# Kernel optimization log

Hardware: AMD Instinct MI355X
Metric: run time of the kernel (lower is better)

The kernel has to match this reference:

```python
import jax, jax.numpy as jnp
import numpy as np

VX, VY, VZ = 0.2, 0.2, 4.0
PCR = (0.0, -40.0, -3.0, 70.4, 40.0, 1.0)
X_OFF = VX / 2 + PCR[0]
Y_OFF = VY / 2 + PCR[1]
Z_OFF = VZ / 2 + PCR[2]
BN_EPS = 1e-3
N_POINTS = 600000
N_VOXELS = 60000
CANVAS_X, CANVAS_Y = 352, 400  # (70.4-0)/0.2, (40-(-40))/0.2


def setup_inputs() -> dict:
    key = jax.random.key(0)
    ks = jax.random.split(key, 8)
    rng = np.random.default_rng(0)
    # pick N_VOXELS distinct occupied voxels on the BEV canvas
    lin = rng.permutation(CANVAS_X * CANVAS_Y)[:N_VOXELS]
    inv = rng.integers(0, N_VOXELS, size=N_POINTS)
    inv[:N_VOXELS] = np.arange(N_VOXELS)  # guarantee every voxel occupied
    pv = lin[inv]
    coors = np.zeros((N_POINTS, 4), np.int32)  # (batch, z, y, x)
    coors[:, 3] = pv % CANVAS_X
    coors[:, 2] = pv // CANVAS_X
    # point features: xyz inside point cloud range + intensity
    px = jax.random.uniform(ks[0], (N_POINTS,), minval=PCR[0], maxval=PCR[3])
    py = jax.random.uniform(ks[1], (N_POINTS,), minval=PCR[1], maxval=PCR[4])
    pz = jax.random.uniform(ks[2], (N_POINTS,), minval=PCR[2], maxval=PCR[5])
    pi = jax.random.uniform(ks[3], (N_POINTS,))
    features = jnp.stack([px, py, pz, pi], axis=1)
    return {
        'features': features,
        'w0': jax.random.normal(ks[4], (10, 64)) * 0.3,
        'g0': jnp.ones((64,)),
        'b0': jnp.zeros((64,)),
        'w1': jax.random.normal(ks[5], (128, 128)) * 0.08,
        'g1': jnp.ones((128,)),
        'b1': jnp.zeros((128,)),
        'coors': jnp.asarray(coors),
        'unq_inv': jnp.asarray(inv.astype(np.int32)),
        'num_voxels': N_VOXELS,
    }


def _bn_relu(x, g, b):
    # BN1d training-mode forward: biased batch stats, eps=1e-3
    mu = jnp.mean(x, axis=0)
    var = jnp.mean(jnp.square(x - mu), axis=0)
    return jax.nn.relu((x - mu) * jax.lax.rsqrt(var + BN_EPS) * g + b)


def reference(features, w0, g0, b0, w1, g1, b1, coors, unq_inv, num_voxels):
    n = features.shape[0]
    cf = coors.astype(features.dtype)
    # cluster center: scatter-mean of point features per voxel, gathered back
    vsum = jax.ops.segment_sum(features, unq_inv, num_segments=num_voxels)
    cnt = jax.ops.segment_sum(jnp.ones((n, 1), features.dtype), unq_inv,
                              num_segments=num_voxels)
    voxel_mean = vsum / jnp.maximum(cnt, 1.0)
    f_cluster = features[:, :3] - voxel_mean[unq_inv][:, :3]
    # offset to voxel center (coors layout: batch, z, y, x)
    f_center = jnp.stack([
        features[:, 0] - (cf[:, 3] * VX + X_OFF),
        features[:, 1] - (cf[:, 2] * VY + Y_OFF),
        features[:, 2] - (cf[:, 1] * VZ + Z_OFF),
    ], axis=1)
    x = jnp.concatenate([features, f_cluster, f_center], axis=1)  # [N,10]
    # VFE layer 0 + scatter-max pool + gather-concat
    p0 = _bn_relu(x @ w0, g0, b0)                                  # [N,64]
    v0 = jax.ops.segment_max(p0, unq_inv, num_segments=num_voxels)
    x1 = jnp.concatenate([p0, v0[unq_inv]], axis=1)                # [N,128]
    # VFE layer 1 + final scatter-max pool
    p1 = _bn_relu(x1 @ w1, g1, b1)                                 # [N,128]
    voxel_feats = jax.ops.segment_max(p1, unq_inv, num_segments=num_voxels)
    return voxel_feats  # [M,128]
```

## Files before the change

kernel.cpp:

```cpp
#include <hip/hip_runtime.h>
#include <hip/hip_bf16.h>


typedef __attribute__((ext_vector_type(8))) short bf16x8;
typedef __attribute__((ext_vector_type(4))) float f32x4;
typedef __attribute__((ext_vector_type(4))) int i32x4;
typedef unsigned short u16;
typedef unsigned int u32;

#define GRIDV 1172
#define RSP 72
#define SCB 2048

__device__ __forceinline__ float bf2f(u16 u) { return __uint_as_float(((u32)u) << 16); }
__device__ __forceinline__ u16 f2bfbits(float f) {
  __hip_bfloat16 h = __float2bfloat16(f);
  return __builtin_bit_cast(u16, h);
}
__device__ __forceinline__ float ldf(const void* p, int i, int flag) {
  return flag ? bf2f(((const u16*)p)[i]) : ((const float*)p)[i];
}
__device__ __forceinline__ u32 encf(float f) {
  u32 b = __float_as_uint(f);
  return b ^ ((u32)(((int)b) >> 31) | 0x80000000u);
}
__device__ __forceinline__ float decf(u32 k) {
  u32 b = (k & 0x80000000u) ? (k ^ 0x80000000u) : ~k;
  return __uint_as_float(b);
}

__device__ __forceinline__ void compute_x(
    int p, const void* __restrict__ feat, const int4* __restrict__ coors4,
    const int* __restrict__ inv, const float* __restrict__ vsum,
    const unsigned* __restrict__ vcnt, int flag, float x[10]) {
  float px, py, pz, pi;
  if (flag) {
    ushort4 f = ((const ushort4*)feat)[p];
    px = bf2f(f.x); py = bf2f(f.y); pz = bf2f(f.z); pi = bf2f(f.w);
  } else {
    float4 f = ((const float4*)feat)[p];
    px = f.x; py = f.y; pz = f.z; pi = f.w;
  }
  int4 c = coors4[p];
  int v = inv[p];
  unsigned cn = vcnt[v];
  float cnt = (float)(cn ? cn : 1u);
  float mx = vsum[3 * v + 0] / cnt;
  float my = vsum[3 * v + 1] / cnt;
  float mz = vsum[3 * v + 2] / cnt;
  x[0] = px; x[1] = py; x[2] = pz; x[3] = pi;
  x[4] = px - mx; x[5] = py - my; x[6] = pz - mz;
  x[7] = px - ((float)c.w * 0.2f + 0.1f);
  x[8] = py - ((float)c.z * 0.2f - 39.9f);
  x[9] = pz - ((float)c.y * 4.0f - 1.0f);
}

__global__ void k_probe(const u32* __restrict__ g0bits, int* __restrict__ flag) {
  if (threadIdx.x == 0 && blockIdx.x == 0)
    flag[0] = (g0bits[0] == 0x3F800000u) ? 0 : 1;
}

__global__ __launch_bounds__(256) void k_pre(
    const void* __restrict__ w0p, const void* __restrict__ w1p,
    const void* __restrict__ g1p,
    u16* __restrict__ w0t, u16* __restrict__ w1t, u32* __restrict__ gsign,
    float4* __restrict__ z4a, long nza4,
    float4* __restrict__ keysws, float4* __restrict__ doutp, long nzk4,
    const int* __restrict__ flagp) {
  const int t = threadIdx.x;
  const int flag = flagp[0];
  if (blockIdx.x == 0) {
    for (int i = t; i < 2048; i += 256) {
      int c = i >> 5, k = i & 31;
      w0t[i] = (k < 10) ? f2bfbits(ldf(w0p, k * 64 + c, flag)) : (u16)0;
    }
    for (int i = t; i < 16384; i += 256) {
      int c = i >> 7, k = i & 127;
      w1t[i] = f2bfbits(ldf(w1p, k * 128 + c, flag));
    }
    if (t < 128) gsign[t] = (ldf(g1p, t, flag) < 0.f) ? 0xFFFFFFFFu : 0u;
  } else {
    float4* keys4 = flag ? keysws : doutp;
    const long total = nza4 + nzk4;
    const long nth = (long)(gridDim.x - 1) * 256;
    const float4 z = {0.f, 0.f, 0.f, 0.f};
    for (long i = (long)(blockIdx.x - 1) * 256 + t; i < total; i += nth) {
      if (i < nza4) z4a[i] = z; else keys4[i - nza4] = z;
    }
  }
}

__global__ __launch_bounds__(256) void k_scatter(
    const void* __restrict__ feat, const int* __restrict__ inv,
    float* __restrict__ vsum, unsigned* __restrict__ vcnt,
    const int* __restrict__ flagp, int n) {
  const int flag = flagp[0];
  const int stride = gridDim.x * blockDim.x;
  for (int p = blockIdx.x * blockDim.x + threadIdx.x; p < n; p += stride) {
    float px, py, pz;
    if (flag) {
      ushort4 f = ((const ushort4*)feat)[p];
      px = bf2f(f.x); py = bf2f(f.y); pz = bf2f(f.z);
    } else {
      float4 f = ((const float4*)feat)[p];
      px = f.x; py = f.y; pz = f.z;
    }
    int v = inv[p];
    atomicAdd(&vsum[3 * v + 0], px);
    atomicAdd(&vsum[3 * v + 1], py);
    atomicAdd(&vsum[3 * v + 2], pz);
    atomicAdd(&vcnt[v], 1u);
  }
}

__global__ __launch_bounds__(256) void k_scanA(const unsigned* __restrict__ vcnt,
                                               unsigned* __restrict__ bsum, int M) {
  __shared__ unsigned sh[4];
  const int t = threadIdx.x;
  long base = (long)blockIdx.x * SCB;
  unsigned s = 0;
  for (int i = t; i < SCB; i += 256) {
    long idx = base + i;
    s += (idx < M) ? vcnt[idx] : 0u;
  }
  #pragma unroll
  for (int off = 1; off < 64; off <<= 1) s += __shfl_xor(s, off);
  if ((t & 63) == 0) sh[t >> 6] = s;
  __syncthreads();
  if (t == 0) bsum[blockIdx.x] = sh[0] + sh[1] + sh[2] + sh[3];
}

__global__ __launch_bounds__(256) void k_scanB(const unsigned* __restrict__ bsum,
                                               unsigned* __restrict__ boff, int nb) {
  __shared__ unsigned sh[256];
  const int t = threadIdx.x;
  unsigned loc[8];
  unsigned s = 0;
  #pragma unroll
  for (int j = 0; j < 8; ++j) {
    int i = t * 8 + j;
    loc[j] = (i < nb) ? bsum[i] : 0u;
    s += loc[j];
  }
  sh[t] = s; __syncthreads();
  for (int off = 1; off < 256; off <<= 1) {
    unsigned add = (t >= off) ? sh[t - off] : 0u;
    __syncthreads();
    sh[t] += add;
    __syncthreads();
  }
  unsigned excl = sh[t] - s;
  #pragma unroll
  for (int j = 0; j < 8; ++j) {
    int i = t * 8 + j;
    if (i < nb) { boff[i] = excl; excl += loc[j]; }
  }
}

__global__ __launch_bounds__(256) void k_scanC(const unsigned* __restrict__ vcnt,
                                               const unsigned* __restrict__ boff,
                                               unsigned* __restrict__ voff, int M) {
  __shared__ unsigned sh[256];
  const int t = threadIdx.x;
  long base = (long)blockIdx.x * SCB;
  unsigned loc[8];
  unsigned s = 0;
  #pragma unroll
  for (int j = 0; j < 8; ++j) {
    long i = base + t * 8 + j;
    loc[j] = (i < M) ? vcnt[i] : 0u;
    s += loc[j];
  }
  sh[t] = s; __syncthreads();
  for (int off = 1; off < 256; off <<= 1) {
    unsigned add = (t >= off) ? sh[t - off] : 0u;
    __syncthreads();
    sh[t] += add;
    __syncthreads();
  }
  unsigned excl = sh[t] - s + boff[blockIdx.x];
  #pragma unroll
  for (int j = 0; j < 8; ++j) {
    long i = base + t * 8 + j;
    if (i < M) { voff[i] = excl; excl += loc[j]; }
  }
}

__global__ __launch_bounds__(256) void k_fillx(
    const void* __restrict__ feat, const int4* __restrict__ coors4,
    const int* __restrict__ inv, const float* __restrict__ vsum,
    const unsigned* __restrict__ vcnt, const unsigned* __restrict__ voff,
    unsigned* __restrict__ wcur, u32* __restrict__ xpk,
    float* __restrict__ stat0acc, const int* __restrict__ flagp, int n) {
  const int flag = flagp[0];
  float acc[65];
  #pragma unroll
  for (int j = 0; j < 65; ++j) acc[j] = 0.f;
  const int t = threadIdx.x;
  const int stride = gridDim.x * blockDim.x;
  for (int p = blockIdx.x * blockDim.x + t; p < n; p += stride) {
    float x[10];
    compute_x(p, feat, coors4, inv, vsum, vcnt, flag, x);
    const int v = inv[p];
    int k = 0;
    #pragma unroll
    for (int a = 0; a < 10; ++a) acc[k++] += x[a];
    #pragma unroll
    for (int a = 0; a < 10; ++a) {
      #pragma unroll
      for (int b = a; b < 10; ++b) acc[k++] += x[a] * x[b];
    }
    u32 u[5];
    #pragma unroll
    for (int j = 0; j < 5; ++j)
      u[j] = (u32)f2bfbits(x[2 * j]) | ((u32)f2bfbits(x[2 * j + 1]) << 16);
    const unsigned pos = voff[v] + atomicAdd(&wcur[v], 1u);
    uint4* dst = (uint4*)(xpk + (long)pos * 8);
    uint4 q0 = {u[0], u[1], u[2], u[3]};
    uint4 q1 = {u[4], (u32)v, 0u, 0u};
    dst[0] = q0;
    dst[1] = q1;
  }
  __shared__ float red[65];
  if (t < 65) red[t] = 0.f;
  __syncthreads();
  const int lane = t & 63;
  #pragma unroll
  for (int j = 0; j < 65; ++j) {
    float s = acc[j];
    #pragma unroll
    for (int off = 1; off < 64; off <<= 1) s += __shfl_xor(s, off);
    if (lane == 0) atomicAdd(&red[j], s);
  }
  __syncthreads();
  if (t < 65) atomicAdd(&stat0acc[t], red[t]);
}

__global__ void k_bn0fin(const float* __restrict__ stat0acc,
                         const void* __restrict__ w0p,
                         const void* __restrict__ g0p,
                         const void* __restrict__ b0p,
                         float* __restrict__ a0, float* __restrict__ c0,
                         const int* __restrict__ flagp, int n) {
  const int flag = flagp[0];
  __shared__ float tot[65];
  const int t = threadIdx.x;
  if (t < 65) tot[t] = stat0acc[t];
  __syncthreads();
  if (t < 64) {
    const float invN = 1.0f / (float)n;
    float w[10];
    #pragma unroll
    for (int i = 0; i < 10; ++i) w[i] = ldf(w0p, i * 64 + t, flag);
    float mu = 0.f;
    #pragma unroll
    for (int i = 0; i < 10; ++i) mu += tot[i] * w[i];
    mu *= invN;
    float e2 = 0.f;
    int k = 10;
    #pragma unroll
    for (int a = 0; a < 10; ++a) {
      #pragma unroll
      for (int b = a; b < 10; ++b) {
        float term = tot[k++] * invN * w[a] * w[b];
        e2 += (a == b) ? term : 2.0f * term;
      }
    }
    float var = fmaxf(e2 - mu * mu, 0.f);
    float rs = 1.0f / sqrtf(var + 1e-3f);
    float aa = ldf(g0p, t, flag) * rs;
    a0[t] = aa;
    c0[t] = ldf(b0p, t, flag) - mu * aa;
  }
}

__device__ __forceinline__ bf16x8 l0frag(const u32* __restrict__ xpk,
                                         long grow, long n, int kg) {
  i32x4 ai = {0, 0, 0, 0};
  if (grow < n) {
    const u32* rp = xpk + grow * 8;
    if (kg == 0) {
      uint4 q = *(const uint4*)rp;
      ai[0] = (int)q.x; ai[1] = (int)q.y; ai[2] = (int)q.z; ai[3] = (int)q.w;
    } else if (kg == 1) {
      ai[0] = (int)rp[4];
    }
  }
  return __builtin_bit_cast(bf16x8, ai);
}

__global__ __launch_bounds__(256) void k_l0vox(
    const u32* __restrict__ xpk, const u16* __restrict__ w0t,
    const float* __restrict__ a0, const float* __restrict__ c0,
    float* __restrict__ v0, int n, int nst, int M) {
  __shared__ float l0stg[4 * 1056];
  __shared__ int vxs[256];
  const int t = threadIdx.x, lane = t & 63, w = t >> 6;
  const int cl = lane & 15, kg = lane >> 4;
  float* fst = l0stg + w * 1056;
  bf16x8 bw[4];
  float al[4], be[4];
  #pragma unroll
  for (int ct = 0; ct < 4; ++ct) {
    bw[ct] = *(const bf16x8*)(w0t + (16 * ct + cl) * 32 + 8 * kg);
    al[ct] = a0[16 * ct + cl];
    be[ct] = c0[16 * ct + cl];
  }
  for (int st = blockIdx.x; st < nst; st += gridDim.x) {
    const long jb = (long)st * 256;
    vxs[t] = (jb + t < n) ? (int)xpk[(jb + t) * 8 + 5] : M;
    int curv = -2;
    float m = 0.f;
    bool edge = true;
    #pragma unroll
    for (int mt = 0; mt < 4; ++mt) {
      const long grow = jb + 64 * w + 16 * mt + cl;
      bf16x8 av = l0frag(xpk, grow, n, kg);
      f32x4 acc[4];
      #pragma unroll
      for (int ct = 0; ct < 4; ++ct) {
        f32x4 z = {0.f, 0.f, 0.f, 0.f};
        acc[ct] = __builtin_amdgcn_mfma_f32_16x16x32_bf16(av, bw[ct], z, 0, 0, 0);
      }
      #pragma unroll
      for (int ct = 0; ct < 4; ++ct)
        #pragma unroll
        for (int i2 = 0; i2 < 4; ++i2)
          fst[(4 * kg + i2) * 66 + 16 * ct + cl] =
              fmaxf(fmaf(acc[ct][i2], al[ct], be[ct]), 0.f);
      const int rbase = 64 * w + 16 * mt;
      for (int r = 0; r < 16; ++r) {
        int v = vxs[rbase + r];
        float a = fst[r * 66 + lane];
        if (v != curv) {
          if (curv >= 0 && curv < M) {
            if (edge) atomicMax((int*)&v0[(long)curv * 64 + lane], __float_as_int(m));
            else      v0[(long)curv * 64 + lane] = m;
          }
          if (curv != -2) edge = false;
          curv = v; m = a;
        } else m = fmaxf(m, a);
      }
    }
    if (curv >= 0 && curv < M)
      atomicMax((int*)&v0[(long)curv * 64 + lane], __float_as_int(m));
  }
}

__device__ __forceinline__ bf16x8 pack8(float4 a, float4 b) {
  bf16x8 r;
  r[0] = (short)f2bfbits(a.x); r[1] = (short)f2bfbits(a.y);
  r[2] = (short)f2bfbits(a.z); r[3] = (short)f2bfbits(a.w);
  r[4] = (short)f2bfbits(b.x); r[5] = (short)f2bfbits(b.y);
  r[6] = (short)f2bfbits(b.z); r[7] = (short)f2bfbits(b.w);
  return r;
}

__global__ __launch_bounds__(256, 2) void k_vfe1vox(
    const u32* __restrict__ xpk, const u16* __restrict__ w0t,
    const float* __restrict__ a0, const float* __restrict__ c0,
    const u16* __restrict__ w1t, const u32* __restrict__ gsign,
    const float* __restrict__ v0,
    u32* __restrict__ keysws, u32* __restrict__ doutk,
    float* __restrict__ stat1acc,
    const int* __restrict__ flagp, int n, int nst, int M) {
  const int flag = flagp[0];
  u32* keys = flag ? keysws : doutk;
  __shared__ u16 stg[256 * RSP];
  __shared__ int vxs[256];
  __shared__ float sred[128], qred[128];
  const int t = threadIdx.x, lane = t & 63, w = t >> 6;
  const int cl = lane & 15, kg = lane >> 4;
  u32* yst = (u32*)(stg + 4608 * w);
  bf16x8 bw[4];
  float al[4], be[4];
  u32 gs[8];
  #pragma unroll
  for (int ct = 0; ct < 4; ++ct) {
    bw[ct] = *(const bf16x8*)(w0t + (16 * ct + cl) * 32 + 8 * kg);
    al[ct] = a0[16 * ct + cl];
    be[ct] = c0[16 * ct + cl];
  }
  #pragma unroll
  for (int ct = 0; ct < 8; ++ct) gs[ct] = gsign[16 * ct + cl];
  float ssum[8], ssq[8];
  #pragma unroll
  for (int jj = 0; jj < 8; ++jj) { ssum[jj] = 0.f; ssq[jj] = 0.f; }
  const f32x4 fz = {0.f, 0.f, 0.f, 0.f};

  for (int st = blockIdx.x; st < nst; st += gridDim.x) {
    const long jb = (long)st * 256;
    vxs[t] = (jb + t < n) ? (int)xpk[(jb + t) * 8 + 5] : M;
    #pragma unroll
    for (int mt = 0; mt < 4; ++mt) {
      const long grow = jb + 64 * w + 16 * mt + cl;
      bf16x8 av = l0frag(xpk, grow, n, kg);
      f32x4 acc0[4];
      #pragma unroll
      for (int ct = 0; ct < 4; ++ct)
        acc0[ct] = __builtin_amdgcn_mfma_f32_16x16x32_bf16(av, bw[ct], fz, 0, 0, 0);
      #pragma unroll
      for (int ct = 0; ct < 4; ++ct) {
        const int c = 16 * ct + cl;
        #pragma unroll
        for (int i2 = 0; i2 < 4; ++i2) {
          const int rloc = 64 * w + 16 * mt + 4 * kg + i2;
          float y = fmaxf(fmaf(acc0[ct][i2], al[ct], be[ct]), 0.f);
          if (jb + rloc >= n) y = 0.f;
          stg[rloc * RSP + c] = f2bfbits(y);
        }
      }
    }
    bf16x8 afr[2][2][4];
    #pragma unroll
    for (int mth = 0; mth < 2; ++mth)
      #pragma unroll
      for (int mtl = 0; mtl < 2; ++mtl) {
        const int rloc = 64 * w + 32 * mth + 16 * mtl + cl;
        afr[mth][mtl][0] = *(const bf16x8*)&stg[rloc * RSP + 8 * kg];
        afr[mth][mtl][1] = *(const bf16x8*)&stg[rloc * RSP + 32 + 8 * kg];
        const int vv = vxs[rloc];
        const float* vr = v0 + (long)vv * 64;
        float4 f0 = *(const float4*)(vr + 8 * kg);
        float4 f1 = *(const float4*)(vr + 8 * kg + 4);
        float4 f2 = *(const float4*)(vr + 32 + 8 * kg);
        float4 f3 = *(const float4*)(vr + 32 + 8 * kg + 4);
        afr[mth][mtl][2] = pack8(f0, f1);
        afr[mth][mtl][3] = pack8(f2, f3);
      }
    int curv = -2;
    u32 m0 = 0, m1 = 0;
    bool edge = true;
    #pragma unroll
    for (int mth = 0; mth < 2; ++mth) {
      f32x4 acc[2][8];
      #pragma unroll
      for (int ct = 0; ct < 8; ++ct) {
        const u16* wr = w1t + (16 * ct + cl) * 128 + 8 * kg;
        bf16x8 b0 = *(const bf16x8*)(wr);
        bf16x8 b1 = *(const bf16x8*)(wr + 32);
        bf16x8 b2 = *(const bf16x8*)(wr + 64);
        bf16x8 b3 = *(const bf16x8*)(wr + 96);
        #pragma unroll
        for (int mtl = 0; mtl < 2; ++mtl) {
          f32x4 a = fz;
          a = __builtin_amdgcn_mfma_f32_16x16x32_bf16(afr[mth][mtl][0], b0, a, 0, 0, 0);
          a = __builtin_amdgcn_mfma_f32_16x16x32_bf16(afr[mth][mtl][1], b1, a, 0, 0, 0);
          a = __builtin_amdgcn_mfma_f32_16x16x32_bf16(afr[mth][mtl][2], b2, a, 0, 0, 0);
          a = __builtin_amdgcn_mfma_f32_16x16x32_bf16(afr[mth][mtl][3], b3, a, 0, 0, 0);
          acc[mtl][ct] = a;
        }
      }
      #pragma unroll
      for (int mtl = 0; mtl < 2; ++mtl) {
        #pragma unroll
        for (int ct = 0; ct < 8; ++ct) {
          #pragma unroll
          for (int i2 = 0; i2 < 4; ++i2) {
            float y = acc[mtl][ct][i2];
            ssum[ct] += y; ssq[ct] += y * y;
            yst[(4 * kg + i2) * 130 + 16 * ct + cl] = encf(y) ^ gs[ct];
          }
        }
        const int rbase = 64 * w + 32 * mth + 16 * mtl;
        for (int r = 0; r < 16; ++r) {
          int v = vxs[rbase + r];
          u32 a0r = yst[r * 130 + lane], a1r = yst[r * 130 + 64 + lane];
          if (v != curv) {
            if (curv >= 0 && curv < M) {
              u32* row = keys + (long)curv * 128;
              if (edge) { atomicMax(&row[lane], m0); atomicMax(&row[64 + lane], m1); }
              else      { row[lane] = m0; row[64 + lane] = m1; }
            }
            if (curv != -2) edge = false;
            curv = v; m0 = a0r; m1 = a1r;
          } else { m0 = max(m0, a0r); m1 = max(m1, a1r); }
        }
      }
    }
    if (curv >= 0 && curv < M) {
      u32* row = keys + (long)curv * 128;
      atomicMax(&row[lane], m0); atomicMax(&row[64 + lane], m1);
    }
  }
  if (t < 128) { sred[t] = 0.f; qred[t] = 0.f; }
  __syncthreads();
  #pragma unroll
  for (int ct = 0; ct < 8; ++ct) {
    float s = ssum[ct], q = ssq[ct];
    s += __shfl_xor(s, 16); s += __shfl_xor(s, 32);
    q += __shfl_xor(q, 16); q += __shfl_xor(q, 32);
    if (lane < 16) {
      atomicAdd(&sred[ct * 16 + cl], s);
      atomicAdd(&qred[ct * 16 + cl], q);
    }
  }
  __syncthreads();
  if (t < 128) {
    atomicAdd(&stat1acc[t], sred[t]);
    atomicAdd(&stat1acc[128 + t], qred[t]);
  }
}

__global__ void k_bn1fin(const float* __restrict__ stat1acc,
                         const void* __restrict__ g1p,
                         const void* __restrict__ b1p,
                         float* __restrict__ a1, float* __restrict__ c1,
                         const int* __restrict__ flagp, int n) {
  const int flag = flagp[0];
  const int c = threadIdx.x;
  float s = stat1acc[c];
  float q = stat1acc[128 + c];
  const float invN = 1.0f / (float)n;
  float mu = s * invN;
  float var = fmaxf(q * invN - mu * mu, 0.f);
  float rs = 1.0f / sqrtf(var + 1e-3f);
  float aa = ldf(g1p, c, flag) * rs;
  a1[c] = aa;
  c1[c] = ldf(b1p, c, flag) - mu * aa;
}

__global__ __launch_bounds__(256) void k_fin(
    const u32* __restrict__ keysws, u32* __restrict__ doutk,
    const float* __restrict__ a1, const float* __restrict__ c1,
    const u32* __restrict__ gsign, void* __restrict__ dout,
    const int* __restrict__ flagp, int m32) {
  const int flag = flagp[0];
  const uint4* src = (const uint4*)(flag ? keysws : doutk);
  const int stride = gridDim.x * blockDim.x;
  for (int i = blockIdx.x * blockDim.x + threadIdx.x; i < m32; i += stride) {
    uint4 k = src[i];
    const int cb = (i * 4) & 127;
    float z0 = fmaxf(fmaf(decf(k.x ^ gsign[cb + 0]), a1[cb + 0], c1[cb + 0]), 0.f);
    float z1 = fmaxf(fmaf(decf(k.y ^ gsign[cb + 1]), a1[cb + 1], c1[cb + 1]), 0.f);
    float z2 = fmaxf(fmaf(decf(k.z ^ gsign[cb + 2]), a1[cb + 2], c1[cb + 2]), 0.f);
    float z3 = fmaxf(fmaf(decf(k.w ^ gsign[cb + 3]), a1[cb + 3], c1[cb + 3]), 0.f);
    if (flag) {
      ushort4 o;
      o.x = f2bfbits(z0); o.y = f2bfbits(z1); o.z = f2bfbits(z2); o.w = f2bfbits(z3);
      ((ushort4*)dout)[i] = o;
    } else {
      float4 o = {z0, z1, z2, z3};
      ((float4*)dout)[i] = o;
    }
  }
}

extern "C" void kernel_launch(void* const* d_in, const int* in_sizes, int n_in,
                              void* d_out, int out_size, void* d_ws, size_t ws_size,
                              hipStream_t stream) {
  (void)n_in; (void)ws_size;
  const int n = in_sizes[0] / 4;
  const int M = out_size / 128;
  const int nst = (n + 255) >> 8;
  const int nb = (M + SCB - 1) / SCB;
  if (n <= 0 || M <= 0) return;

  const void* feat = d_in[0];
  const void* w0p = d_in[1];
  const void* g0p = d_in[2];
  const void* b0p = d_in[3];
  const void* w1p = d_in[4];
  const void* g1p = d_in[5];
  const void* b1p = d_in[6];
  const int4* coors4 = (const int4*)d_in[7];
  const int* inv = (const int*)d_in[8];

  char* wsb = (char*)d_ws;
  long off = 0;
  auto alloc = [&](long bytes) -> void* {
    void* p = wsb + off;
    off = (off + bytes + 255) & ~255L;
    return p;
  };
  int* flagp = (int*)alloc(256);
  float* a0 = (float*)alloc(256);
  float* c0 = (float*)alloc(256);
  float* a1 = (float*)alloc(512);
  float* c1 = (float*)alloc(512);
  u32* gsign = (u32*)alloc(512);
  u16* w0t = (u16*)alloc(2048 * 2);
  u16* w1t = (u16*)alloc(16384 * 2);
  unsigned* bsum = (unsigned*)alloc(2048 * 4);
  unsigned* boff = (unsigned*)alloc(2048 * 4);
  unsigned* voff = (unsigned*)alloc((long)M * 4);
  u32* xpk = (u32*)alloc((long)nst * 256 * 32);
  const long nza = 384L + 3L * M + M + (long)(M + 1) * 64 + M;
  float* zbase = (float*)alloc(((nza + 3) / 4) * 16);
  float* stat0acc = zbase;
  float* stat1acc = zbase + 80;
  float* vsum = zbase + 384;
  unsigned* vcnt = (unsigned*)(vsum + 3L * M);
  float* v0 = (float*)(vcnt + M);
  unsigned* wcur = (unsigned*)(v0 + (long)(M + 1) * 64);
  u32* keysws = (u32*)alloc((long)M * 128 * 4);

  hipLaunchKernelGGL(k_probe, dim3(1), dim3(64), 0, stream, (const u32*)g0p, flagp);
  hipLaunchKernelGGL(k_pre, dim3(2048), dim3(256), 0, stream,
                     w0p, w1p, g1p, w0t, w1t, gsign,
                     (float4*)zbase, (nza + 3) / 4,
                     (float4*)keysws, (float4*)d_out, (long)M * 32, flagp);
  hipLaunchKernelGGL(k_scatter, dim3(1024), dim3(256), 0, stream, feat, inv, vsum, vcnt, flagp, n);
  hipLaunchKernelGGL(k_scanA, dim3(nb), dim3(256), 0, stream, vcnt, bsum, M);
  hipLaunchKernelGGL(k_scanB, dim3(1), dim3(256), 0, stream, bsum, boff, nb);
  hipLaunchKernelGGL(k_scanC, dim3(nb), dim3(256), 0, stream, vcnt, boff, voff, M);
  hipLaunchKernelGGL(k_fillx, dim3(1024), dim3(256), 0, stream,
                     feat, coors4, inv, vsum, vcnt, voff, wcur, xpk, stat0acc, flagp, n);
  hipLaunchKernelGGL(k_bn0fin, dim3(1), dim3(128), 0, stream,
                     stat0acc, w0p, g0p, b0p, a0, c0, flagp, n);
  hipLaunchKernelGGL(k_l0vox, dim3(GRIDV), dim3(256), 0, stream,
                     xpk, w0t, a0, c0, v0, n, nst, M);
  hipLaunchKernelGGL(k_vfe1vox, dim3(GRIDV), dim3(256), 0, stream,
                     xpk, w0t, a0, c0, w1t, gsign, v0,
                     keysws, (u32*)d_out, stat1acc, flagp, n, nst, M);
  hipLaunchKernelGGL(k_bn1fin, dim3(1), dim3(128), 0, stream,
                     stat1acc, g1p, b1p, a1, c1, flagp, n);
  hipLaunchKernelGGL(k_fin, dim3(1024), dim3(256), 0, stream,
                     keysws, (u32*)d_out, a1, c1, gsign, d_out, flagp, M * 32);
}
```

Measured before the change: 435.6 us.

## Replace float atomic voxel sums with sorted gather and merge block-edge maxima in shared memory

The per-point float atomicAdd scatter for voxel sums is replaced by a count histogram, a fill pass that builds a sorted point list plus a point-to-position map, and a per-voxel gather that sums features without atomics. fillx reuses the precomputed positions instead of doing a second atomic slot claim. The two VFE kernels now give each wave a fixed run of contiguous 64-row segments instead of grid-striding over 256-row tiles. Each wave's boundary voxels are merged across the block in shared memory, so fewer global atomicMax calls are needed, and vfe1vox occupancy is raised to 3 blocks. The cost is two extra launches and extra workspace traffic, and the per-voxel serial gather loop is unbalanced because voxel point counts vary.

```diff
diff --git a/kernel.cpp b/kernel.cpp
--- a/kernel.cpp
+++ b/kernel.cpp
@@ -8,9 +8,11 @@
 typedef unsigned short u16;
 typedef unsigned int u32;
 
-#define GRIDV 1172
 #define RSP 72
 #define SCB 2048
+#define WPB 4
+#define SPW0 2
+#define SPW1 3
 
 __device__ __forceinline__ float bf2f(u16 u) { return __uint_as_float(((u32)u) << 16); }
 __device__ __forceinline__ u16 f2bfbits(float f) {
@@ -90,27 +92,11 @@
   }
 }
 
-__global__ __launch_bounds__(256) void k_scatter(
-    const void* __restrict__ feat, const int* __restrict__ inv,
-    float* __restrict__ vsum, unsigned* __restrict__ vcnt,
-    const int* __restrict__ flagp, int n) {
-  const int flag = flagp[0];
+__global__ __launch_bounds__(256) void k_hist(const int* __restrict__ inv,
+                                              unsigned* __restrict__ vcnt, int n) {
   const int stride = gridDim.x * blockDim.x;
-  for (int p = blockIdx.x * blockDim.x + threadIdx.x; p < n; p += stride) {
-    float px, py, pz;
-    if (flag) {
-      ushort4 f = ((const ushort4*)feat)[p];
-      px = bf2f(f.x); py = bf2f(f.y); pz = bf2f(f.z);
-    } else {
-      float4 f = ((const float4*)feat)[p];
-      px = f.x; py = f.y; pz = f.z;
-    }
-    int v = inv[p];
-    atomicAdd(&vsum[3 * v + 0], px);
-    atomicAdd(&vsum[3 * v + 1], py);
-    atomicAdd(&vsum[3 * v + 2], pz);
-    atomicAdd(&vcnt[v], 1u);
-  }
+  for (int p = blockIdx.x * blockDim.x + threadIdx.x; p < n; p += stride)
+    atomicAdd(&vcnt[inv[p]], 1u);
 }
 
 __global__ __launch_bounds__(256) void k_scanA(const unsigned* __restrict__ vcnt,
@@ -186,12 +172,49 @@
   }
 }
 
+__global__ __launch_bounds__(256) void k_fill(
+    const int* __restrict__ inv, const unsigned* __restrict__ voff,
+    unsigned* __restrict__ wcur, int* __restrict__ plist,
+    unsigned* __restrict__ pt2pos, int n) {
+  const int stride = gridDim.x * blockDim.x;
+  for (int p = blockIdx.x * blockDim.x + threadIdx.x; p < n; p += stride) {
+    int v = inv[p];
+    unsigned pos = voff[v] + atomicAdd(&wcur[v], 1u);
+    plist[pos] = p;
+    pt2pos[p] = pos;
+  }
+}
+
+__global__ __launch_bounds__(256) void k_vsum(
+    const void* __restrict__ feat, const int* __restrict__ plist,
+    const unsigned* __restrict__ voff, const unsigned* __restrict__ vcnt,
+    float* __restrict__ vsum, const int* __restrict__ flagp, int M) {
+  const int flag = flagp[0];
+  const int v = blockIdx.x * 256 + threadIdx.x;
+  if (v >= M) return;
+  const unsigned o = voff[v], c = vcnt[v];
+  float sx = 0.f, sy = 0.f, sz = 0.f;
+  for (unsigned j = 0; j < c; ++j) {
+    int pid = plist[o + j];
+    if (flag) {
+      ushort4 f = ((const ushort4*)feat)[pid];
+      sx += bf2f(f.x); sy += bf2f(f.y); sz += bf2f(f.z);
+    } else {
+      float4 f = ((const float4*)feat)[pid];
+      sx += f.x; sy += f.y; sz += f.z;
+    }
+  }
+  vsum[3 * v + 0] = sx;
+  vsum[3 * v + 1] = sy;
+  vsum[3 * v + 2] = sz;
+}
+
 __global__ __launch_bounds__(256) void k_fillx(
     const void* __restrict__ feat, const int4* __restrict__ coors4,
     const int* __restrict__ inv, const float* __restrict__ vsum,
-    const unsigned* __restrict__ vcnt, const unsigned* __restrict__ voff,
-    unsigned* __restrict__ wcur, u32* __restrict__ xpk,
-    float* __restrict__ stat0acc, const int* __restrict__ flagp, int n) {
+    const unsigned* __restrict__ vcnt, const unsigned* __restrict__ pt2pos,
+    u32* __restrict__ xpk, float* __restrict__ stat0acc,
+    const int* __restrict__ flagp, int n) {
   const int flag = flagp[0];
   float acc[65];
   #pragma unroll
@@ -214,7 +237,7 @@
     #pragma unroll
     for (int j = 0; j < 5; ++j)
       u[j] = (u32)f2bfbits(x[2 * j]) | ((u32)f2bfbits(x[2 * j + 1]) << 16);
-    const unsigned pos = voff[v] + atomicAdd(&wcur[v], 1u);
+    const unsigned pos = pt2pos[p];
     uint4* dst = (uint4*)(xpk + (long)pos * 8);
     uint4 q0 = {u[0], u[1], u[2], u[3]};
     uint4 q1 = {u[4], (u32)v, 0u, 0u};
@@ -292,9 +315,11 @@
 __global__ __launch_bounds__(256) void k_l0vox(
     const u32* __restrict__ xpk, const u16* __restrict__ w0t,
     const float* __restrict__ a0, const float* __restrict__ c0,
-    float* __restrict__ v0, int n, int nst, int M) {
+    float* __restrict__ v0, long n, long nseg, int M) {
   __shared__ float l0stg[4 * 1056];
-  __shared__ int vxs[256];
+  __shared__ int vxsw[4][64];
+  __shared__ float pval[8][64];
+  __shared__ int pvox[8];
   const int t = threadIdx.x, lane = t & 63, w = t >> 6;
   const int cl = lane & 15, kg = lane >> 4;
   float* fst = l0stg + w * 1056;
@@ -306,15 +331,17 @@
     al[ct] = a0[16 * ct + cl];
     be[ct] = c0[16 * ct + cl];
   }
-  for (int st = blockIdx.x; st < nst; st += gridDim.x) {
-    const long jb = (long)st * 256;
-    vxs[t] = (jb + t < n) ? (int)xpk[(jb + t) * 8 + 5] : M;
-    int curv = -2;
-    float m = 0.f;
-    bool edge = true;
+  int curv = -2; float m = 0.f;
+  bool first = true; int fvox = -2; float fm = 0.f;
+  const long seg0 = ((long)blockIdx.x * WPB + w) * SPW0;
+  for (int s = 0; s < SPW0; ++s) {
+    const long seg = seg0 + s;
+    if (seg >= nseg) break;
+    const long jb = seg * 64;
+    vxsw[w][lane] = (jb + lane < n) ? (int)xpk[(jb + lane) * 8 + 5] : M;
     #pragma unroll
     for (int mt = 0; mt < 4; ++mt) {
-      const long grow = jb + 64 * w + 16 * mt + cl;
+      const long grow = jb + 16 * mt + cl;
       bf16x8 av = l0frag(xpk, grow, n, kg);
       f32x4 acc[4];
       #pragma unroll
@@ -328,22 +355,40 @@
         for (int i2 = 0; i2 < 4; ++i2)
           fst[(4 * kg + i2) * 66 + 16 * ct + cl] =
               fmaxf(fmaf(acc[ct][i2], al[ct], be[ct]), 0.f);
-      const int rbase = 64 * w + 16 * mt;
+      const int rb = 16 * mt;
       for (int r = 0; r < 16; ++r) {
-        int v = vxs[rbase + r];
+        int v = vxsw[w][rb + r];
         float a = fst[r * 66 + lane];
         if (v != curv) {
           if (curv >= 0 && curv < M) {
-            if (edge) atomicMax((int*)&v0[(long)curv * 64 + lane], __float_as_int(m));
-            else      v0[(long)curv * 64 + lane] = m;
+            if (first) { fvox = curv; fm = m; first = false; }
+            else v0[(long)curv * 64 + lane] = m;
           }
-          if (curv != -2) edge = false;
           curv = v; m = a;
         } else m = fmaxf(m, a);
       }
     }
-    if (curv >= 0 && curv < M)
-      atomicMax((int*)&v0[(long)curv * 64 + lane], __float_as_int(m));
+  }
+  if (lane == 0) { pvox[2 * w] = fvox; pvox[2 * w + 1] = curv; }
+  pval[2 * w][lane] = fm;
+  pval[2 * w + 1][lane] = m;
+  __syncthreads();
+  if (t < 64) {
+    int vox = -2; float val = 0.f; bool afirst = true;
+    for (int e = 0; e < 8; ++e) {
+      int ev = pvox[e];
+      if (ev < 0 || ev >= M) continue;
+      float evv = pval[e][t];
+      if (ev == vox) val = fmaxf(val, evv);
+      else {
+        if (vox >= 0) {
+          if (afirst) { atomicMax((int*)&v0[(long)vox * 64 + t], __float_as_int(val)); afirst = false; }
+          else v0[(long)vox * 64 + t] = val;
+        }
+        vox = ev; val = evv;
+      }
+    }
+    if (vox >= 0) atomicMax((int*)&v0[(long)vox * 64 + t], __float_as_int(val));
   }
 }
 
@@ -356,19 +401,21 @@
   return r;
 }
 
-__global__ __launch_bounds__(256, 2) void k_vfe1vox(
+__global__ __launch_bounds__(256, 3) void k_vfe1vox(
     const u32* __restrict__ xpk, const u16* __restrict__ w0t,
     const float* __restrict__ a0, const float* __restrict__ c0,
     const u16* __restrict__ w1t, const u32* __restrict__ gsign,
     const float* __restrict__ v0,
     u32* __restrict__ keysws, u32* __restrict__ doutk,
     float* __restrict__ stat1acc,
-    const int* __restrict__ flagp, int n, int nst, int M) {
+    const int* __restrict__ flagp, long n, long nseg, int M) {
   const int flag = flagp[0];
   u32* keys = flag ? keysws : doutk;
   __shared__ u16 stg[256 * RSP];
-  __shared__ int vxs[256];
+  __shared__ int vxsw[4][64];
   __shared__ float sred[128], qred[128];
+  __shared__ u32 pval[8][128];
+  __shared__ int pvox[8];
   const int t = threadIdx.x, lane = t & 63, w = t >> 6;
   const int cl = lane & 15, kg = lane >> 4;
   u32* yst = (u32*)(stg + 4608 * w);
@@ -388,12 +435,18 @@
   for (int jj = 0; jj < 8; ++jj) { ssum[jj] = 0.f; ssq[jj] = 0.f; }
   const f32x4 fz = {0.f, 0.f, 0.f, 0.f};
 
-  for (int st = blockIdx.x; st < nst; st += gridDim.x) {
-    const long jb = (long)st * 256;
-    vxs[t] = (jb + t < n) ? (int)xpk[(jb + t) * 8 + 5] : M;
+  int curv = -2; u32 m0 = 0, m1 = 0;
+  bool first = true; int fvox = -2; u32 fm0 = 0, fm1 = 0;
+  const long seg0 = ((long)blockIdx.x * WPB + w) * SPW1;
+
+  for (int s = 0; s < SPW1; ++s) {
+    const long seg = seg0 + s;
+    if (seg >= nseg) break;
+    const long jb = seg * 64;
+    vxsw[w][lane] = (jb + lane < n) ? (int)xpk[(jb + lane) * 8 + 5] : M;
     #pragma unroll
     for (int mt = 0; mt < 4; ++mt) {
-      const long grow = jb + 64 * w + 16 * mt + cl;
+      const long grow = jb + 16 * mt + cl;
       bf16x8 av = l0frag(xpk, grow, n, kg);
       f32x4 acc0[4];
       #pragma unroll
@@ -404,10 +457,10 @@
         const int c = 16 * ct + cl;
         #pragma unroll
         for (int i2 = 0; i2 < 4; ++i2) {
-          const int rloc = 64 * w + 16 * mt + 4 * kg + i2;
+          const int lr = 16 * mt + 4 * kg + i2;
           float y = fmaxf(fmaf(acc0[ct][i2], al[ct], be[ct]), 0.f);
-          if (jb + rloc >= n) y = 0.f;
-          stg[rloc * RSP + c] = f2bfbits(y);
+          if (jb + lr >= n) y = 0.f;
+          stg[(64 * w + lr) * RSP + c] = f2bfbits(y);
         }
       }
     }
@@ -416,10 +469,10 @@
     for (int mth = 0; mth < 2; ++mth)
       #pragma unroll
       for (int mtl = 0; mtl < 2; ++mtl) {
-        const int rloc = 64 * w + 32 * mth + 16 * mtl + cl;
-        afr[mth][mtl][0] = *(const bf16x8*)&stg[rloc * RSP + 8 * kg];
-        afr[mth][mtl][1] = *(const bf16x8*)&stg[rloc * RSP + 32 + 8 * kg];
-        const int vv = vxs[rloc];
+        const int lr = 32 * mth + 16 * mtl + cl;
+        afr[mth][mtl][0] = *(const bf16x8*)&stg[(64 * w + lr) * RSP + 8 * kg];
+        afr[mth][mtl][1] = *(const bf16x8*)&stg[(64 * w + lr) * RSP + 32 + 8 * kg];
+        const int vv = vxsw[w][lr];
         const float* vr = v0 + (long)vv * 64;
         float4 f0 = *(const float4*)(vr + 8 * kg);
         float4 f1 = *(const float4*)(vr + 8 * kg + 4);
@@ -428,9 +481,6 @@
         afr[mth][mtl][2] = pack8(f0, f1);
         afr[mth][mtl][3] = pack8(f2, f3);
       }
-    int curv = -2;
-    u32 m0 = 0, m1 = 0;
-    bool edge = true;
     #pragma unroll
     for (int mth = 0; mth < 2; ++mth) {
       f32x4 acc[2][8];
@@ -462,29 +512,46 @@
             yst[(4 * kg + i2) * 130 + 16 * ct + cl] = encf(y) ^ gs[ct];
           }
         }
-        const int rbase = 64 * w + 32 * mth + 16 * mtl;
+        const int rb = 32 * mth + 16 * mtl;
         for (int r = 0; r < 16; ++r) {
-          int v = vxs[rbase + r];
+          int v = vxsw[w][rb + r];
           u32 a0r = yst[r * 130 + lane], a1r = yst[r * 130 + 64 + lane];
           if (v != curv) {
             if (curv >= 0 && curv < M) {
-              u32* row = keys + (long)curv * 128;
-              if (edge) { atomicMax(&row[lane], m0); atomicMax(&row[64 + lane], m1); }
-              else      { row[lane] = m0; row[64 + lane] = m1; }
+              if (first) { fvox = curv; fm0 = m0; fm1 = m1; first = false; }
+              else {
+                u32* row = keys + (long)curv * 128;
+                row[lane] = m0; row[64 + lane] = m1;
+              }
             }
-            if (curv != -2) edge = false;
             curv = v; m0 = a0r; m1 = a1r;
           } else { m0 = max(m0, a0r); m1 = max(m1, a1r); }
         }
       }
     }
-    if (curv >= 0 && curv < M) {
-      u32* row = keys + (long)curv * 128;
-      atomicMax(&row[lane], m0); atomicMax(&row[64 + lane], m1);
-    }
-  }
+  }
+  if (lane == 0) { pvox[2 * w] = fvox; pvox[2 * w + 1] = curv; }
+  pval[2 * w][lane] = fm0; pval[2 * w][64 + lane] = fm1;
+  pval[2 * w + 1][lane] = m0; pval[2 * w + 1][64 + lane] = m1;
   if (t < 128) { sred[t] = 0.f; qred[t] = 0.f; }
   __syncthreads();
+  if (t < 128) {
+    int vox = -2; u32 val = 0; bool afirst = true;
+    for (int e = 0; e < 8; ++e) {
+      int ev = pvox[e];
+      if (ev < 0 || ev >= M) continue;
+      u32 evv = pval[e][t];
+      if (ev == vox) val = max(val, evv);
+      else {
+        if (vox >= 0) {
+          if (afirst) { atomicMax(&keys[(long)vox * 128 + t], val); afirst = false; }
+          else keys[(long)vox * 128 + t] = val;
+        }
+        vox = ev; val = evv;
+      }
+    }
+    if (vox >= 0) atomicMax(&keys[(long)vox * 128 + t], val);
+  }
   #pragma unroll
   for (int ct = 0; ct < 8; ++ct) {
     float s = ssum[ct], q = ssq[ct];
@@ -552,8 +619,11 @@
   (void)n_in; (void)ws_size;
   const int n = in_sizes[0] / 4;
   const int M = out_size / 128;
-  const int nst = (n + 255) >> 8;
+  const long nseg = (n + 63) >> 6;
   const int nb = (M + SCB - 1) / SCB;
+  const int nblk0 = (int)((nseg + WPB * SPW0 - 1) / (WPB * SPW0));
+  const int nblk1 = (int)((nseg + WPB * SPW1 - 1) / (WPB * SPW1));
+  const int nbv = (M + 255) / 256;
   if (n <= 0 || M <= 0) return;
 
   const void* feat = d_in[0];
@@ -584,13 +654,15 @@
   unsigned* bsum = (unsigned*)alloc(2048 * 4);
   unsigned* boff = (unsigned*)alloc(2048 * 4);
   unsigned* voff = (unsigned*)alloc((long)M * 4);
-  u32* xpk = (u32*)alloc((long)nst * 256 * 32);
-  const long nza = 384L + 3L * M + M + (long)(M + 1) * 64 + M;
+  float* vsum = (float*)alloc((long)M * 3 * 4);
+  int* plist = (int*)alloc((long)nseg * 64 * 4);
+  unsigned* pt2pos = (unsigned*)alloc((long)n * 4);
+  u32* xpk = (u32*)alloc((long)nseg * 64 * 32);
+  const long nza = 384L + M + (long)(M + 1) * 64 + M;
   float* zbase = (float*)alloc(((nza + 3) / 4) * 16);
   float* stat0acc = zbase;
   float* stat1acc = zbase + 80;
-  float* vsum = zbase + 384;
-  unsigned* vcnt = (unsigned*)(vsum + 3L * M);
+  unsigned* vcnt = (unsigned*)(zbase + 384);
   float* v0 = (float*)(vcnt + M);
   unsigned* wcur = (unsigned*)(v0 + (long)(M + 1) * 64);
   u32* keysws = (u32*)alloc((long)M * 128 * 4);
@@ -600,19 +672,23 @@
                      w0p, w1p, g1p, w0t, w1t, gsign,
                      (float4*)zbase, (nza + 3) / 4,
                      (float4*)keysws, (float4*)d_out, (long)M * 32, flagp);
-  hipLaunchKernelGGL(k_scatter, dim3(1024), dim3(256), 0, stream, feat, inv, vsum, vcnt, flagp, n);
+  hipLaunchKernelGGL(k_hist, dim3(1024), dim3(256), 0, stream, inv, vcnt, n);
   hipLaunchKernelGGL(k_scanA, dim3(nb), dim3(256), 0, stream, vcnt, bsum, M);
   hipLaunchKernelGGL(k_scanB, dim3(1), dim3(256), 0, stream, bsum, boff, nb);
   hipLaunchKernelGGL(k_scanC, dim3(nb), dim3(256), 0, stream, vcnt, boff, voff, M);
+  hipLaunchKernelGGL(k_fill, dim3(1024), dim3(256), 0, stream,
+                     inv, voff, wcur, plist, pt2pos, n);
+  hipLaunchKernelGGL(k_vsum, dim3(nbv), dim3(256), 0, stream,
+                     feat, plist, voff, vcnt, vsum, flagp, M);
   hipLaunchKernelGGL(k_fillx, dim3(1024), dim3(256), 0, stream,
-                     feat, coors4, inv, vsum, vcnt, voff, wcur, xpk, stat0acc, flagp, n);
+                     feat, coors4, inv, vsum, vcnt, pt2pos, xpk, stat0acc, flagp, n);
   hipLaunchKernelGGL(k_bn0fin, dim3(1), dim3(128), 0, stream,
                      stat0acc, w0p, g0p, b0p, a0, c0, flagp, n);
-  hipLaunchKernelGGL(k_l0vox, dim3(GRIDV), dim3(256), 0, stream,
-                     xpk, w0t, a0, c0, v0, n, nst, M);
-  hipLaunchKernelGGL(k_vfe1vox, dim3(GRIDV), dim3(256), 0, stream,
+  hipLaunchKernelGGL(k_l0vox, dim3(nblk0), dim3(256), 0, stream,
+                     xpk, w0t, a0, c0, v0, (long)n, nseg, M);
+  hipLaunchKernelGGL(k_vfe1vox, dim3(nblk1), dim3(256), 0, stream,
                      xpk, w0t, a0, c0, w1t, gsign, v0,
-                     keysws, (u32*)d_out, stat1acc, flagp, n, nst, M);
+                     keysws, (u32*)d_out, stat1acc, flagp, (long)n, nseg, M);
   hipLaunchKernelGGL(k_bn1fin, dim3(1), dim3(128), 0, stream,
                      stat1acc, g1p, b1p, a1, c1, flagp, n);
   hipLaunchKernelGGL(k_fin, dim3(1024), dim3(256), 0, stream,
```

New measurement: 499.7 us. +14.7%, slower.
